# Kernel tuning notes

Hardware: AMD Instinct MI355X
Metric: run time of the kernel (lower is better)

Reference implementation:

```python
import jax, jax.numpy as jnp
import numpy as np

NUM_NODES = 2048
NUM_REL = 8
HIDDEN = 256


def setup_inputs() -> dict:
    key = jax.random.key(0)
    k1, k2, k3 = jax.random.split(key, 3)
    X = jax.random.normal(k1, (NUM_NODES, HIDDEN, NUM_REL), dtype=jnp.float32)
    A = jax.random.uniform(k2, (NUM_NODES, NUM_NODES, NUM_REL), dtype=jnp.float32)
    # nn.init.normal_(std=0.01)
    weight = 0.01 * jax.random.normal(k3, (HIDDEN, HIDDEN, NUM_REL), dtype=jnp.float32)
    return {"X": X, "A": A, "weight": weight}


def _tensor_product(A, B):
    # Faithful to the original: FFT along last (relation) dim, take REAL part of
    # both transformed operands, per-slice matmul, then real part of ifft.
    Af = jnp.real(jnp.fft.fft(A, axis=-1))  # (n1, n2, k)
    Bf = jnp.real(jnp.fft.fft(B, axis=-1))  # (n2, n4, k)
    C = jnp.einsum('nmk,mhk->nhk', Af, Bf)  # batched real matmul over slices k
    return jnp.real(jnp.fft.ifft(C, axis=-1)).astype(A.dtype)


def reference(X, A, weight):
    res = _tensor_product(A, X)          # (num_nodes, hidden, num_rel)
    res = _tensor_product(res, weight)   # (num_nodes, hidden, num_rel)
    return res
```

## Files before the change

### kernel.cpp

```cpp
#include <hip/hip_runtime.h>


typedef __bf16 bf16_t;
typedef __bf16 bf16x2 __attribute__((ext_vector_type(2)));
typedef __bf16 bf16x8 __attribute__((ext_vector_type(8)));
typedef float f32x4 __attribute__((ext_vector_type(4)));

#define R2C 0.70710678118654752f

__device__ __forceinline__ size_t swz(int r, int c, int K) {
  return (size_t)r * K + (c & ~63) + ((((c >> 3) & 7) ^ (r & 7)) << 3) + (c & 7);
}

__device__ __forceinline__ void async_cp16(const void* g, void* l) {
  __builtin_amdgcn_global_load_lds((const __attribute__((address_space(1))) char*)g,
                                   (__attribute__((address_space(3))) char*)l,
                                   16, 0, 0);
}

__device__ __forceinline__ void fwd5(const float x[8], float F[5]) {
  float s04 = x[0] + x[4], d04 = x[0] - x[4];
  float s26 = x[2] + x[6];
  float s15 = x[1] + x[5], s37 = x[3] + x[7];
  float t = (x[1] + x[7]) - (x[3] + x[5]);
  float e = s04 + s26, o = s15 + s37;
  F[0] = e + o;
  F[1] = d04 + R2C * t;
  F[2] = s04 - s26;
  F[3] = d04 - R2C * t;
  F[4] = e - o;
}

__global__ __launch_bounds__(256) void k_pre(const float* __restrict__ X,
                                             const float* __restrict__ A,
                                             const float* __restrict__ W,
                                             bf16_t* __restrict__ Xft,
                                             bf16_t* __restrict__ Af,
                                             bf16_t* __restrict__ Wft) {
  __shared__ bf16_t tx[40][256];
  int b = blockIdx.x;
  if (b < 8192) {
    size_t t = (size_t)b * 256 + threadIdx.x;
    size_t idx = t * 2;
    int n = (int)(idx >> 11), m = (int)(idx & 2047);
    const float4* p = (const float4*)(A + idx * 8);
    float4 q0 = p[0], q1 = p[1], q2 = p[2], q3 = p[3];
    float x0[8] = {q0.x, q0.y, q0.z, q0.w, q1.x, q1.y, q1.z, q1.w};
    float x1[8] = {q2.x, q2.y, q2.z, q2.w, q3.x, q3.y, q3.z, q3.w};
    float F0[5], F1[5];
    fwd5(x0, F0);
    fwd5(x1, F1);
    size_t pos = swz(n, m, 2048);
#pragma unroll
    for (int j = 0; j < 5; j++) {
      bf16x2 v = {(bf16_t)F0[j], (bf16_t)F1[j]};
      *(bf16x2*)(Af + (size_t)j * 4194304 + pos) = v;
    }
  } else if (b < 8448) {
    int bx = b - 8192;
    int m0 = (bx & 7) * 256, h0 = (bx >> 3) * 8;
    int t = threadIdx.x;
    const float4* p = (const float4*)(X + (((size_t)(m0 + t) * 256) + h0) * 8);
#pragma unroll
    for (int h = 0; h < 8; h++) {
      float4 a = p[2 * h], bb = p[2 * h + 1];
      float x[8] = {a.x, a.y, a.z, a.w, bb.x, bb.y, bb.z, bb.w};
      float F[5];
      fwd5(x, F);
#pragma unroll
      for (int j = 0; j < 5; j++) tx[j * 8 + h][t] = (bf16_t)F[j];
    }
    __syncthreads();
#pragma unroll
    for (int it = 0; it < 5; it++) {
      int slot = it * 256 + t;
      int row = slot >> 5, ch = slot & 31;
      int j = row >> 3, hl = row & 7;
      int h = h0 + hl;
      size_t gpos = (size_t)j * 524288 + (size_t)h * 2048 + m0 +
                    ((ch & ~7) << 3) + (((ch & 7) ^ (h & 7)) << 3);
      *(uint4*)(Xft + gpos) = *(const uint4*)(&tx[row][ch * 8]);
    }
  } else {
    int h = b - 8448;
    int hp = threadIdx.x;
    const float4* p = (const float4*)(W + ((size_t)hp * 256 + h) * 8);
    float4 a = p[0], bb = p[1];
    float x[8] = {a.x, a.y, a.z, a.w, bb.x, bb.y, bb.z, bb.w};
    float F[5];
    fwd5(x, F);
    const float sc[5] = {0.125f, 0.25f, 0.25f, 0.25f, 0.125f};
    size_t pos = swz(h, hp, 256);
#pragma unroll
    for (int j = 0; j < 5; j++)
      Wft[(size_t)j * 65536 + pos] = (bf16_t)(F[j] * sc[j]);
  }
}

template <typename OutT, bool SWZ_OUT>
__global__ __launch_bounds__(256) void gemm_lds(const bf16_t* __restrict__ A,
                                                const bf16_t* __restrict__ B,
                                                OutT* __restrict__ C, int K,
                                                size_t ap, size_t bp, size_t cp) {
  __shared__ bf16_t sm[4 * 8192];
  const int j = blockIdx.z;
  const bf16_t* Aj = A + (size_t)j * ap;
  const bf16_t* Bj = B + (size_t)j * bp;
  OutT* Cj = C + (size_t)j * cp;
  const int n0 = blockIdx.x * 128, h0 = blockIdx.y * 128;
  const int tid = threadIdx.x;
  const int wv = tid >> 6, ln = tid & 63;
  const int quad = ln >> 4, l16 = ln & 15;
  const int wn = (wv & 1) * 64, wh = (wv >> 1) * 64;

  const bf16_t* ga[4];
  const bf16_t* gb[4];
  int lo[4];
#pragma unroll
  for (int s = 0; s < 4; s++) {
    int slot = s * 256 + tid;
    int row = slot >> 3, c16 = slot & 7;
    ga[s] = Aj + (size_t)(n0 + row) * K + c16 * 8;
    gb[s] = Bj + (size_t)(h0 + row) * K + c16 * 8;
    lo[s] = (s * 256 + wv * 64) * 8;
  }

#pragma unroll
  for (int s = 0; s < 4; s++) {
    async_cp16(ga[s], sm + lo[s]);
    async_cp16(gb[s], sm + 16384 + lo[s]);
  }

  f32x4 acc[4][4] = {};
  for (int kk = 0; kk < K; kk += 64) {
    int p = (kk >> 6) & 1;
    if (kk + 64 < K) {
#pragma unroll
      for (int s = 0; s < 4; s++) {
        async_cp16(ga[s] + kk + 64, sm + (p ^ 1) * 8192 + lo[s]);
        async_cp16(gb[s] + kk + 64, sm + 16384 + (p ^ 1) * 8192 + lo[s]);
      }
      __builtin_amdgcn_s_waitcnt(0xF78);
    } else {
      __builtin_amdgcn_s_waitcnt(0xF70);
    }
    __builtin_amdgcn_s_barrier();
    const bf16_t* Asp = sm + p * 8192;
    const bf16_t* Bsp = sm + 16384 + p * 8192;
#pragma unroll
    for (int kh = 0; kh < 2; kh++) {
      bf16x8 af[4], bfr[4];
      int c16 = kh * 4 + quad;
#pragma unroll
      for (int i = 0; i < 4; i++) {
        int ra = wn + i * 16 + l16;
        int rb = wh + i * 16 + l16;
        af[i] = *(const bf16x8*)(Asp + ra * 64 + ((c16 ^ (ra & 7)) << 3));
        bfr[i] = *(const bf16x8*)(Bsp + rb * 64 + ((c16 ^ (rb & 7)) << 3));
      }
#pragma unroll
      for (int i = 0; i < 4; i++)
#pragma unroll
        for (int t = 0; t < 4; t++)
          acc[i][t] = __builtin_amdgcn_mfma_f32_16x16x32_bf16(af[i], bfr[t],
                                                              acc[i][t], 0, 0, 0);
    }
    __builtin_amdgcn_s_barrier();
  }
#pragma unroll
  for (int i = 0; i < 4; i++) {
#pragma unroll
    for (int t = 0; t < 4; t++) {
      int hc = h0 + wh + t * 16 + l16;
#pragma unroll
      for (int rg = 0; rg < 4; rg++) {
        int nr = n0 + wn + i * 16 + quad * 4 + rg;
        size_t off = SWZ_OUT ? swz(nr, hc, 256) : (size_t)nr * 256 + hc;
        Cj[off] = (OutT)acc[i][t][rg];
      }
    }
  }
}

__global__ __launch_bounds__(256) void k_combine(const float* __restrict__ C2,
                                                 float* __restrict__ out) {
  size_t idx = (size_t)blockIdx.x * 256 + threadIdx.x;
  float c0 = C2[idx];
  float c1 = C2[524288 + idx];
  float c2 = C2[2 * 524288 + idx];
  float c3 = C2[3 * 524288 + idx];
  float c4 = C2[4 * 524288 + idx];
  float o0 = c0 + c1 + c2 + c3 + c4;
  float o4 = c0 - c1 + c2 - c3 + c4;
  float o2 = c0 - c2 + c4;
  float rt = R2C * (c1 - c3);
  float o1 = c0 + rt - c4;
  float o3 = c0 - rt - c4;
  float4* op = (float4*)(out + idx * 8);
  op[0] = make_float4(o0, o1, o2, o3);
  op[1] = make_float4(o4, o3, o2, o1);
}

extern "C" void kernel_launch(void* const* d_in, const int* in_sizes, int n_in,
                              void* d_out, int out_size, void* d_ws, size_t ws_size,
                              hipStream_t stream) {
  const float* X = (const float*)d_in[0];
  const float* A = (const float*)d_in[1];
  const float* W = (const float*)d_in[2];
  float* out = (float*)d_out;
  char* ws = (char*)d_ws;

  bf16_t* Af  = (bf16_t*)(ws);
  bf16_t* Xft = (bf16_t*)(ws + 41943040);
  bf16_t* Wft = (bf16_t*)(ws + 47185920);
  bf16_t* C1  = (bf16_t*)(ws + 47841280);
  float*  C2  = (float*) (ws + 53084160);

  k_pre<<<dim3(8704), 256, 0, stream>>>(X, A, W, Xft, Af, Wft);
  gemm_lds<bf16_t, true><<<dim3(16, 2, 5), 256, 0, stream>>>(
      Af, Xft, C1, 2048, (size_t)4194304, (size_t)524288, (size_t)524288);
  gemm_lds<float, false><<<dim3(16, 2, 5), 256, 0, stream>>>(
      C1, Wft, C2, 256, (size_t)524288, (size_t)65536, (size_t)524288);
  k_combine<<<dim3(2048), 256, 0, stream>>>(C2, out);
}
```

Baseline: 256.4 us.

## Fold inverse DFT into second GEMM via expanded weight matrix, drop combine kernel

The preprocessing kernel now builds an expanded weight matrix with the inverse-DFT cosine coefficients baked in, laid out as 2048x1280. The first GEMM writes its five frequency slices side by side into one 2048x1280 activation matrix. A single second GEMM with K=1280 then writes the final interleaved output directly. This removes the fp32 C2 round trip and the k_combine launch. In exchange the second GEMM does several times more MFMA work and its weight matrix is larger.

Result: slower. 261.7 us (+2.0%).

```diff
diff --git a/kernel.cpp b/kernel.cpp
--- a/kernel.cpp
+++ b/kernel.cpp
@@ -36,7 +36,7 @@
                                              const float* __restrict__ W,
                                              bf16_t* __restrict__ Xft,
                                              bf16_t* __restrict__ Af,
-                                             bf16_t* __restrict__ Wft) {
+                                             bf16_t* __restrict__ Wbig) {
   __shared__ bf16_t tx[40][256];
   int b = blockIdx.x;
   if (b < 8192) {
@@ -90,10 +90,24 @@
     float F[5];
     fwd5(x, F);
     const float sc[5] = {0.125f, 0.25f, 0.25f, 0.25f, 0.125f};
-    size_t pos = swz(h, hp, 256);
-#pragma unroll
-    for (int j = 0; j < 5; j++)
-      Wft[(size_t)j * 65536 + pos] = (bf16_t)(F[j] * sc[j]);
+    const float CK[8][5] = {
+        {1.f, 1.f, 1.f, 1.f, 1.f},
+        {1.f, R2C, 0.f, -R2C, -1.f},
+        {1.f, 0.f, -1.f, 0.f, 1.f},
+        {1.f, -R2C, 0.f, R2C, -1.f},
+        {1.f, -1.f, 1.f, -1.f, 1.f},
+        {1.f, -R2C, 0.f, R2C, -1.f},
+        {1.f, 0.f, -1.f, 0.f, 1.f},
+        {1.f, R2C, 0.f, -R2C, -1.f}};
+#pragma unroll
+    for (int k = 0; k < 8; k++) {
+      int c = h * 8 + k;
+      size_t base = (size_t)c * 1280 + (hp & ~63) +
+                    ((((hp >> 3) & 7) ^ (c & 7)) << 3) + (hp & 7);
+#pragma unroll
+      for (int j = 0; j < 5; j++)
+        Wbig[base + (size_t)j * 256] = (bf16_t)(F[j] * sc[j] * CK[k][j]);
+    }
   }
 }
 
@@ -101,7 +115,8 @@
 __global__ __launch_bounds__(256) void gemm_lds(const bf16_t* __restrict__ A,
                                                 const bf16_t* __restrict__ B,
                                                 OutT* __restrict__ C, int K,
-                                                size_t ap, size_t bp, size_t cp) {
+                                                int ldc, size_t ap, size_t bp,
+                                                size_t cp) {
   __shared__ bf16_t sm[4 * 8192];
   const int j = blockIdx.z;
   const bf16_t* Aj = A + (size_t)j * ap;
@@ -175,30 +190,11 @@
 #pragma unroll
       for (int rg = 0; rg < 4; rg++) {
         int nr = n0 + wn + i * 16 + quad * 4 + rg;
-        size_t off = SWZ_OUT ? swz(nr, hc, 256) : (size_t)nr * 256 + hc;
+        size_t off = SWZ_OUT ? swz(nr, hc, ldc) : (size_t)nr * ldc + hc;
         Cj[off] = (OutT)acc[i][t][rg];
       }
     }
   }
-}
-
-__global__ __launch_bounds__(256) void k_combine(const float* __restrict__ C2,
-                                                 float* __restrict__ out) {
-  size_t idx = (size_t)blockIdx.x * 256 + threadIdx.x;
-  float c0 = C2[idx];
-  float c1 = C2[524288 + idx];
-  float c2 = C2[2 * 524288 + idx];
-  float c3 = C2[3 * 524288 + idx];
-  float c4 = C2[4 * 524288 + idx];
-  float o0 = c0 + c1 + c2 + c3 + c4;
-  float o4 = c0 - c1 + c2 - c3 + c4;
-  float o2 = c0 - c2 + c4;
-  float rt = R2C * (c1 - c3);
-  float o1 = c0 + rt - c4;
-  float o3 = c0 - rt - c4;
-  float4* op = (float4*)(out + idx * 8);
-  op[0] = make_float4(o0, o1, o2, o3);
-  op[1] = make_float4(o4, o3, o2, o1);
 }
 
 extern "C" void kernel_launch(void* const* d_in, const int* in_sizes, int n_in,
@@ -210,16 +206,14 @@
   float* out = (float*)d_out;
   char* ws = (char*)d_ws;
 
-  bf16_t* Af  = (bf16_t*)(ws);
-  bf16_t* Xft = (bf16_t*)(ws + 41943040);
-  bf16_t* Wft = (bf16_t*)(ws + 47185920);
-  bf16_t* C1  = (bf16_t*)(ws + 47841280);
-  float*  C2  = (float*) (ws + 53084160);
-
-  k_pre<<<dim3(8704), 256, 0, stream>>>(X, A, W, Xft, Af, Wft);
+  bf16_t* Af   = (bf16_t*)(ws);
+  bf16_t* Xft  = (bf16_t*)(ws + 41943040);
+  bf16_t* Wbig = (bf16_t*)(ws + 47185920);
+  bf16_t* C1   = (bf16_t*)(ws + 52428800);
+
+  k_pre<<<dim3(8704), 256, 0, stream>>>(X, A, W, Xft, Af, Wbig);
   gemm_lds<bf16_t, true><<<dim3(16, 2, 5), 256, 0, stream>>>(
-      Af, Xft, C1, 2048, (size_t)4194304, (size_t)524288, (size_t)524288);
-  gemm_lds<float, false><<<dim3(16, 2, 5), 256, 0, stream>>>(
-      C1, Wft, C2, 256, (size_t)524288, (size_t)65536, (size_t)524288);
-  k_combine<<<dim3(2048), 256, 0, stream>>>(C2, out);
-}
+      Af, Xft, C1, 2048, 1280, (size_t)4194304, (size_t)524288, (size_t)256);
+  gemm_lds<float, false><<<dim3(16, 16, 1), 256, 0, stream>>>(
+      C1, Wbig, out, 1280, 2048, (size_t)0, (size_t)0, (size_t)0);
+}
```

## Deepen first GEMM to 4-stage LDS ring and load full K in second

Applied to the files above, without the earlier changes.

The first batched GEMM (K=2048) moves from a 2-stage double buffer to a 4-slot LDS ring with three tiles in flight, using finer vmcnt waits, so more global-load latency is hidden. The second GEMM (K=256) becomes a specialized kernel that loads the whole 128x256 A and B tiles into LDS at once, then runs all MFMAs after a single barrier, removing the per-step barriers. Both kernels now use 128 KB of LDS per block, which limits occupancy to one block per CU. The grid is only 160 blocks, so the workload is latency-bound.

Result: no change. 256.8 us (+0.2%).

```diff
diff --git a/kernel.cpp b/kernel.cpp
--- a/kernel.cpp
+++ b/kernel.cpp
@@ -97,16 +97,15 @@
   }
 }
 
-template <typename OutT, bool SWZ_OUT>
-__global__ __launch_bounds__(256) void gemm_lds(const bf16_t* __restrict__ A,
-                                                const bf16_t* __restrict__ B,
-                                                OutT* __restrict__ C, int K,
-                                                size_t ap, size_t bp, size_t cp) {
-  __shared__ bf16_t sm[4 * 8192];
+__global__ __launch_bounds__(256) void gemm_ring(const bf16_t* __restrict__ A,
+                                                 const bf16_t* __restrict__ B,
+                                                 bf16_t* __restrict__ C, int K,
+                                                 size_t ap, size_t bp, size_t cp) {
+  __shared__ bf16_t sm[65536];
   const int j = blockIdx.z;
   const bf16_t* Aj = A + (size_t)j * ap;
   const bf16_t* Bj = B + (size_t)j * bp;
-  OutT* Cj = C + (size_t)j * cp;
+  bf16_t* Cj = C + (size_t)j * cp;
   const int n0 = blockIdx.x * 128, h0 = blockIdx.y * 128;
   const int tid = threadIdx.x;
   const int wv = tid >> 6, ln = tid & 63;
@@ -125,28 +124,37 @@
     lo[s] = (s * 256 + wv * 64) * 8;
   }
 
-#pragma unroll
-  for (int s = 0; s < 4; s++) {
-    async_cp16(ga[s], sm + lo[s]);
-    async_cp16(gb[s], sm + 16384 + lo[s]);
+  const int T = K >> 6;
+#pragma unroll
+  for (int i = 0; i < 3; i++) {
+#pragma unroll
+    for (int s = 0; s < 4; s++) {
+      async_cp16(ga[s] + i * 64, sm + i * 8192 + lo[s]);
+      async_cp16(gb[s] + i * 64, sm + 32768 + i * 8192 + lo[s]);
+    }
   }
 
   f32x4 acc[4][4] = {};
-  for (int kk = 0; kk < K; kk += 64) {
-    int p = (kk >> 6) & 1;
-    if (kk + 64 < K) {
+  for (int t = 0; t < T; t++) {
+    int b = t & 3;
+    if (t + 3 < T) {
+      int nb = (t + 3) & 3;
 #pragma unroll
       for (int s = 0; s < 4; s++) {
-        async_cp16(ga[s] + kk + 64, sm + (p ^ 1) * 8192 + lo[s]);
-        async_cp16(gb[s] + kk + 64, sm + 16384 + (p ^ 1) * 8192 + lo[s]);
-      }
+        async_cp16(ga[s] + (t + 3) * 64, sm + nb * 8192 + lo[s]);
+        async_cp16(gb[s] + (t + 3) * 64, sm + 32768 + nb * 8192 + lo[s]);
+      }
+      __builtin_amdgcn_s_waitcnt(0x4F78);
+    } else if (t + 2 < T) {
+      __builtin_amdgcn_s_waitcnt(0x4F70);
+    } else if (t + 1 < T) {
       __builtin_amdgcn_s_waitcnt(0xF78);
     } else {
       __builtin_amdgcn_s_waitcnt(0xF70);
     }
     __builtin_amdgcn_s_barrier();
-    const bf16_t* Asp = sm + p * 8192;
-    const bf16_t* Bsp = sm + 16384 + p * 8192;
+    const bf16_t* Asp = sm + b * 8192;
+    const bf16_t* Bsp = sm + 32768 + b * 8192;
 #pragma unroll
     for (int kh = 0; kh < 2; kh++) {
       bf16x8 af[4], bfr[4];
@@ -161,9 +169,9 @@
 #pragma unroll
       for (int i = 0; i < 4; i++)
 #pragma unroll
-        for (int t = 0; t < 4; t++)
-          acc[i][t] = __builtin_amdgcn_mfma_f32_16x16x32_bf16(af[i], bfr[t],
-                                                              acc[i][t], 0, 0, 0);
+        for (int t2 = 0; t2 < 4; t2++)
+          acc[i][t2] = __builtin_amdgcn_mfma_f32_16x16x32_bf16(af[i], bfr[t2],
+                                                               acc[i][t2], 0, 0, 0);
     }
     __builtin_amdgcn_s_barrier();
   }
@@ -175,8 +183,67 @@
 #pragma unroll
       for (int rg = 0; rg < 4; rg++) {
         int nr = n0 + wn + i * 16 + quad * 4 + rg;
-        size_t off = SWZ_OUT ? swz(nr, hc, 256) : (size_t)nr * 256 + hc;
-        Cj[off] = (OutT)acc[i][t][rg];
+        Cj[swz(nr, hc, 256)] = (bf16_t)acc[i][t][rg];
+      }
+    }
+  }
+}
+
+__global__ __launch_bounds__(256) void gemm_flat(const bf16_t* __restrict__ A,
+                                                 const bf16_t* __restrict__ B,
+                                                 float* __restrict__ C) {
+  __shared__ bf16_t sm[65536];
+  const int j = blockIdx.z;
+  const bf16_t* Aj = A + (size_t)j * 524288;
+  const bf16_t* Bj = B + (size_t)j * 65536;
+  float* Cj = C + (size_t)j * 524288;
+  const int n0 = blockIdx.x * 128, h0 = blockIdx.y * 128;
+  const int tid = threadIdx.x;
+  const int wv = tid >> 6, ln = tid & 63;
+  const int quad = ln >> 4, l16 = ln & 15;
+  const int wn = (wv & 1) * 64, wh = (wv >> 1) * 64;
+
+#pragma unroll
+  for (int s = 0; s < 16; s++) {
+    int st = s * 256 + tid;
+    int row = st >> 5, c = st & 31;
+    int lo = (s * 256 + wv * 64) * 8;
+    async_cp16(Aj + (size_t)(n0 + row) * 256 + c * 8, sm + lo);
+    async_cp16(Bj + (size_t)(h0 + row) * 256 + c * 8, sm + 32768 + lo);
+  }
+  __builtin_amdgcn_s_waitcnt(0xF70);
+  __builtin_amdgcn_s_barrier();
+
+  f32x4 acc[4][4] = {};
+#pragma unroll
+  for (int kh = 0; kh < 8; kh++) {
+    bf16x8 af[4], bfr[4];
+    int c16 = kh * 4 + quad;
+    int cb = (c16 & ~7) << 3;
+#pragma unroll
+    for (int i = 0; i < 4; i++) {
+      int ra = wn + i * 16 + l16;
+      int rb = wh + i * 16 + l16;
+      af[i] = *(const bf16x8*)(sm + ra * 256 + cb + (((c16 & 7) ^ (ra & 7)) << 3));
+      bfr[i] = *(const bf16x8*)(sm + 32768 + rb * 256 + cb +
+                                (((c16 & 7) ^ (rb & 7)) << 3));
+    }
+#pragma unroll
+    for (int i = 0; i < 4; i++)
+#pragma unroll
+      for (int t = 0; t < 4; t++)
+        acc[i][t] = __builtin_amdgcn_mfma_f32_16x16x32_bf16(af[i], bfr[t],
+                                                            acc[i][t], 0, 0, 0);
+  }
+#pragma unroll
+  for (int i = 0; i < 4; i++) {
+#pragma unroll
+    for (int t = 0; t < 4; t++) {
+      int hc = h0 + wh + t * 16 + l16;
+#pragma unroll
+      for (int rg = 0; rg < 4; rg++) {
+        int nr = n0 + wn + i * 16 + quad * 4 + rg;
+        Cj[(size_t)nr * 256 + hc] = acc[i][t][rg];
       }
     }
   }
@@ -217,9 +284,8 @@
   float*  C2  = (float*) (ws + 53084160);
 
   k_pre<<<dim3(8704), 256, 0, stream>>>(X, A, W, Xft, Af, Wft);
-  gemm_lds<bf16_t, true><<<dim3(16, 2, 5), 256, 0, stream>>>(
+  gemm_ring<<<dim3(16, 2, 5), 256, 0, stream>>>(
       Af, Xft, C1, 2048, (size_t)4194304, (size_t)524288, (size_t)524288);
-  gemm_lds<float, false><<<dim3(16, 2, 5), 256, 0, stream>>>(
-      C1, Wft, C2, 256, (size_t)524288, (size_t)65536, (size_t)524288);
+  gemm_flat<<<dim3(16, 2, 5), 256, 0, stream>>>(C1, Wft, C2);
   k_combine<<<dim3(2048), 256, 0, stream>>>(C2, out);
 }
```
